# Performance work log

Measured on AMD Instinct MI355X. Metric: run time of the kernel, lower is better.

## Reference

```python
import jax, jax.numpy as jnp
import numpy as np

N_GRAPHS = 512  # number of graphs in the batch (static for segment_sum)


def _gcn_norm(edge_index, n_nodes):
    # PyG GCNConv default: add self-loops, symmetric normalization D^-1/2 (A+I) D^-1/2
    loop = jnp.arange(n_nodes, dtype=edge_index.dtype)
    row = jnp.concatenate([edge_index[0], loop])  # source nodes
    col = jnp.concatenate([edge_index[1], loop])  # target nodes
    deg = jax.ops.segment_sum(jnp.ones_like(col, dtype=jnp.float32), col,
                              num_segments=n_nodes)
    dinv = jnp.where(deg > 0, jax.lax.rsqrt(jnp.maximum(deg, 1.0)), 0.0)
    norm = dinv[row] * dinv[col]  # [E + N]
    return row, col, norm


def _gcn_conv(x, row, col, norm, W, b):
    n_nodes = x.shape[0]
    h = x @ W                                   # [N, H] transform first (small GEMM)
    msg = h[row] * norm[:, None]                # gather + scale: [E+N, H]
    out = jax.ops.segment_sum(msg, col, num_segments=n_nodes)  # scatter-add
    return out + b


def _global_mean_pool(h, batch, n_graphs):
    sums = jax.ops.segment_sum(h, batch, num_segments=n_graphs)
    cnt = jax.ops.segment_sum(jnp.ones((h.shape[0],), h.dtype), batch,
                              num_segments=n_graphs)
    return sums / jnp.maximum(cnt, 1.0)[:, None]


def setup_inputs() -> dict:
    key = jax.random.key(0)
    ks = jax.random.split(key, 12)
    N, E, D, H, G, F = 100000, 1600000, 128, 128, N_GRAPHS, 1
    s_in = 1.0 / np.sqrt(D)
    s_h = 1.0 / np.sqrt(H)
    s_5h = 1.0 / np.sqrt(5 * H)
    return {
        "x": jax.random.normal(ks[0], (N, D), dtype=jnp.float32),
        "edge_index": jax.random.randint(ks[1], (2, E), 0, N, dtype=jnp.int64
                                         if jax.config.jax_enable_x64 else jnp.int32),
        "batch": jnp.sort(jax.random.randint(ks[2], (N,), 0, G, dtype=jnp.int64
                                             if jax.config.jax_enable_x64 else jnp.int32)),
        "W1": jax.random.normal(ks[3], (D, H), jnp.float32) * s_in,
        "b1": jnp.zeros((H,), jnp.float32),
        "W2": jax.random.normal(ks[4], (H, H), jnp.float32) * s_h,
        "b2": jnp.zeros((H,), jnp.float32),
        "W3": jax.random.normal(ks[5], (H, H), jnp.float32) * s_h,
        "b3": jnp.zeros((H,), jnp.float32),
        "W4": jax.random.normal(ks[6], (H, H), jnp.float32) * s_h,
        "b4": jnp.zeros((H,), jnp.float32),
        "Wl1": jax.random.normal(ks[7], (5 * H, 5 * H), jnp.float32) * s_5h,
        "bl1": jnp.zeros((5 * H,), jnp.float32),
        "Wl2": jax.random.normal(ks[8], (5 * H, F), jnp.float32) * s_5h,
        "bl2": jnp.zeros((F,), jnp.float32),
    }


def reference(x, edge_index, batch, W1, b1, W2, b2, W3, b3, W4, b4,
              Wl1, bl1, Wl2, bl2):
    n_nodes = x.shape[0]
    row, col, norm = _gcn_norm(edge_index, n_nodes)
    h1 = jax.nn.relu(_gcn_conv(x, row, col, norm, W1, b1))
    h2 = jax.nn.relu(_gcn_conv(h1, row, col, norm, W2, b2))
    h3 = jax.nn.relu(_gcn_conv(h2, row, col, norm, W3, b3))
    h4 = jax.nn.relu(_gcn_conv(h3, row, col, norm, W4, b4))
    # NOTE: source applies conv4 twice (h5 uses self.conv4); conv5 is unused.
    h5 = jax.nn.relu(_gcn_conv(h4, row, col, norm, W4, b4))
    p = jnp.concatenate([
        _global_mean_pool(h1, batch, N_GRAPHS),
        _global_mean_pool(h2, batch, N_GRAPHS),
        _global_mean_pool(h3, batch, N_GRAPHS),
        _global_mean_pool(h4, batch, N_GRAPHS),
        _global_mean_pool(h5, batch, N_GRAPHS),
    ], axis=1)                                   # [G, 5H]
    h = jax.nn.relu(p @ Wl1 + bl1)
    # dropout p=0.5 is identity in eval mode
    h = h @ Wl2 + bl2                            # [G, F]
    return h.reshape(-1)
```

## Files before the change

kernel.cpp:

```cpp
#include <hip/hip_runtime.h>
#include <hip/hip_fp16.h>

#define HID 128

__device__ __forceinline__ float bf2f(unsigned short u) {
    union { unsigned int i; float f; } v;
    v.i = ((unsigned int)u) << 16;
    return v.f;
}
__device__ __forceinline__ unsigned short f2bf(float f) {
    union { float f; unsigned int i; } v;
    v.f = f;
    unsigned int lsb = (v.i >> 16) & 1u;
    v.i += 0x7fffu + lsb;
    return (unsigned short)(v.i >> 16);
}

template <int S>
__device__ __forceinline__ float fp8_dec(unsigned int v) {
#if __has_builtin(__builtin_amdgcn_cvt_f32_fp8)
    return __builtin_amdgcn_cvt_f32_fp8(v, S);
#else
    unsigned int b = (v >> (S * 8)) & 0xffu;
    unsigned short u = (unsigned short)(((b & 0x80u) << 8) | ((b & 0x7fu) << 7));
    return __half2float(__ushort_as_half(u)) * 256.0f;
#endif
}
__device__ __forceinline__ unsigned char fp8_enc(float f) {
    f = fminf(fmaxf(f, -448.f), 448.f);
    unsigned short u = __half_as_ushort(__float2half(f * 0.00390625f));
    unsigned short r = (unsigned short)(u + (((u >> 7) & 1u) + 0x3fu));
    return (unsigned char)(((r >> 7) & 0x7fu) | ((u >> 8) & 0x80u));
}

typedef __attribute__((ext_vector_type(8))) short bf16x8;
typedef __attribute__((ext_vector_type(4))) float f32x4;

__global__ void k_prep(const int* __restrict__ col, int* __restrict__ degI,
                       int* __restrict__ rank,
                       const float* __restrict__ W1, const float* __restrict__ W2,
                       const float* __restrict__ W3, const float* __restrict__ W4,
                       unsigned short* __restrict__ Wg,
                       const int* __restrict__ batch, int* __restrict__ gstart,
                       int E, int N, int G, int degGrid) {
    int bid = blockIdx.x;
    if (bid < degGrid) {
        int i = bid * 256 + threadIdx.x;
        if (i < E) rank[i] = atomicAdd(&degI[col[i]], 1);
        return;
    }
    bid -= degGrid;
    if (bid < 256) {
        int m = bid >> 6;
        int i = (bid & 63) * 256 + threadIdx.x;
        const float* Wm = (m == 0) ? W1 : (m == 1) ? W2 : (m == 2) ? W3 : W4;
        int k = i >> 7, n = i & 127;
        int ks = k >> 5, q = (k >> 3) & 3, j = k & 7;
        int ct = n >> 4, c = n & 15;
        Wg[m * 16384 + ((((ks * 8 + ct) * 4 + q) * 16 + c) << 3) + j] = f2bf(Wm[i]);
        return;
    }
    bid -= 256;
    int g = bid * 256 + threadIdx.x;
    if (g > G) return;
    int lo = 0, hi = N;
    while (lo < hi) {
        int mid = (lo + hi) >> 1;
        if (batch[mid] < g) lo = mid + 1; else hi = mid;
    }
    gstart[g] = lo;
}

__global__ void k_scan_part(const int* __restrict__ degI, int* __restrict__ partial,
                            int* __restrict__ sums, int N) {
    __shared__ int sh[1024];
    int tid = threadIdx.x;
    int i = blockIdx.x * 1024 + tid;
    int v = (i < N) ? (degI[i] + 1) : 0;
    sh[tid] = v;
    __syncthreads();
    for (int off = 1; off < 1024; off <<= 1) {
        int t = (tid >= off) ? sh[tid - off] : 0;
        __syncthreads();
        sh[tid] += t;
        __syncthreads();
    }
    if (i < N) partial[i] = sh[tid] - v;
    if (tid == 1023) sums[blockIdx.x] = sh[1023];
}
__global__ void k_scan_tops(int* __restrict__ sums, int* __restrict__ indptr,
                            int nblocks, int N) {
    __shared__ int sh[1024];
    int tid = threadIdx.x;
    int v = (tid < nblocks) ? sums[tid] : 0;
    sh[tid] = v;
    __syncthreads();
    for (int off = 1; off < 1024; off <<= 1) {
        int t = (tid >= off) ? sh[tid - off] : 0;
        __syncthreads();
        sh[tid] += t;
        __syncthreads();
    }
    if (tid < nblocks) sums[tid] = sh[tid] - v;
    if (tid == 1023) indptr[N] = sh[1023];
}
__global__ void k_scan_fix(const int* __restrict__ partial, const int* __restrict__ sums,
                           const int* __restrict__ degI, int* __restrict__ indptr,
                           float* __restrict__ dinv, int N) {
    int i = blockIdx.x * blockDim.x + threadIdx.x;
    if (i < N) {
        indptr[i] = partial[i] + sums[i >> 10];
        dinv[i] = 1.0f / sqrtf((float)(degI[i] + 1));
    }
}

__device__ __forceinline__ bf16x8 a_frag_load(const unsigned short* p) {
    return *(const bf16x8*)p;
}
__device__ __forceinline__ bf16x8 a_frag_load(const float* p) {
    bf16x8 r;
#pragma unroll
    for (int i = 0; i < 8; ++i) r[i] = (short)f2bf(p[i]);
    return r;
}

template <typename TA>
__device__ __forceinline__ void gemm_body(const TA* __restrict__ A,
                                          const unsigned short* __restrict__ B,
                                          unsigned char* __restrict__ C,
                                          int N, int blk) {
    const int tid = threadIdx.x;
    const int lane = tid & 63, wave = tid >> 6;
    const int q = lane >> 4, c = lane & 15;
    const int rowBase = blk * 128 + wave * 32;

    f32x4 acc[2][8];
#pragma unroll
    for (int rt = 0; rt < 2; ++rt)
#pragma unroll
        for (int ct = 0; ct < 8; ++ct)
            acc[rt][ct] = (f32x4){0.f, 0.f, 0.f, 0.f};

    const bf16x8 zfrag = {};
#pragma unroll
    for (int ks = 0; ks < 4; ++ks) {
        bf16x8 a[2];
#pragma unroll
        for (int rt = 0; rt < 2; ++rt) {
            int r = rowBase + rt * 16 + c;
            a[rt] = (r < N) ? a_frag_load(A + (size_t)r * HID + ks * 32 + q * 8)
                            : zfrag;
        }
#pragma unroll
        for (int ct = 0; ct < 8; ++ct) {
            bf16x8 b = *(const bf16x8*)&B[((((ks * 8 + ct) * 4 + q) * 16 + c) << 3)];
            acc[0][ct] = __builtin_amdgcn_mfma_f32_16x16x32_bf16(a[0], b, acc[0][ct], 0, 0, 0);
            acc[1][ct] = __builtin_amdgcn_mfma_f32_16x16x32_bf16(a[1], b, acc[1][ct], 0, 0, 0);
        }
    }
#pragma unroll
    for (int rt = 0; rt < 2; ++rt)
#pragma unroll
        for (int reg = 0; reg < 4; ++reg) {
            int r = rowBase + rt * 16 + q * 4 + reg;
            if (r < N) {
#pragma unroll
                for (int ct = 0; ct < 8; ++ct)
                    C[(size_t)r * HID + ct * 16 + c] = fp8_enc(acc[rt][ct][reg]);
            }
        }
}

__device__ __forceinline__ void pool_body(const unsigned short* __restrict__ h,
                                          const int* __restrict__ gstart,
                                          float* __restrict__ pbuf,
                                          int layer, int g, int lane) {
    int s = gstart[g], e = gstart[g + 1];
    float sx[4] = {0.f, 0.f, 0.f, 0.f};
    float sy[4] = {0.f, 0.f, 0.f, 0.f};
    int v = s;
    for (; v + 7 < e; v += 8) {
        unsigned int pk[8];
#pragma unroll
        for (int u = 0; u < 8; ++u)
            pk[u] = ((const unsigned int*)(h + (size_t)(v + u) * HID))[lane];
#pragma unroll
        for (int u = 0; u < 8; ++u) {
            sx[u & 3] += bf2f((unsigned short)(pk[u] & 0xffffu));
            sy[u & 3] += bf2f((unsigned short)(pk[u] >> 16));
        }
    }
    for (; v < e; ++v) {
        unsigned int pk = ((const unsigned int*)(h + (size_t)v * HID))[lane];
        sx[0] += bf2f((unsigned short)(pk & 0xffffu));
        sy[0] += bf2f((unsigned short)(pk >> 16));
    }
    float inv = 1.0f / fmaxf((float)(e - s), 1.0f);
    float ox = ((sx[0] + sx[1]) + (sx[2] + sx[3])) * inv;
    float oy = ((sy[0] + sy[1]) + (sy[2] + sy[3])) * inv;
    float* dst = pbuf + (size_t)g * 640 + layer * HID + lane * 2;
    dst[0] = ox;
    dst[1] = oy;
}

__global__ __launch_bounds__(256) void k_fused0(const float* __restrict__ x,
                                                const unsigned short* __restrict__ Wg,
                                                unsigned char* __restrict__ buf0,
                                                const int* __restrict__ row,
                                                const int* __restrict__ col,
                                                const float* __restrict__ dinv,
                                                const int* __restrict__ indptr,
                                                const int* __restrict__ rank,
                                                int2* __restrict__ adj,
                                                int E, int N, int gemmGrid) {
    __shared__ unsigned short Wsw[16384];
    if (blockIdx.x < gemmGrid) {
        const uint4* src = (const uint4*)Wg;
        uint4* dst = (uint4*)Wsw;
        for (int i = threadIdx.x; i < 2048; i += 256) dst[i] = src[i];
        __syncthreads();
        gemm_body<float>(x, Wsw, buf0, N, blockIdx.x);
        return;
    }
    int e = (blockIdx.x - gemmGrid) * blockDim.x + threadIdx.x;
    if (e >= E + N) return;
    int s, d, p;
    if (e < E) { s = row[e]; d = col[e]; p = indptr[d] + rank[e]; }
    else       { s = d = e - E; p = indptr[d + 1] - 1; }
    adj[p] = make_int2(s, __float_as_int(dinv[s] * dinv[d]));
}

__global__ __launch_bounds__(256) void k_gemm_pool(const unsigned short* __restrict__ A,
                                                   const unsigned short* __restrict__ Wg,
                                                   unsigned char* __restrict__ C,
                                                   int N,
                                                   const int* __restrict__ gstart,
                                                   float* __restrict__ pbuf,
                                                   int poolLayer, int G, int gemmGrid) {
    if (blockIdx.x < gemmGrid) {
        gemm_body<unsigned short>(A, Wg, C, N, blockIdx.x);
        return;
    }
    int g = (blockIdx.x - gemmGrid) * 4 + (threadIdx.x >> 6);
    if (g >= G) return;
    pool_body(A, gstart, pbuf, poolLayer, g, threadIdx.x & 63);
}

__global__ __launch_bounds__(256) void k_aggregate(const unsigned char* __restrict__ t,
                                                   const int* __restrict__ indptr,
                                                   const int2* __restrict__ adj,
                                                   const float* __restrict__ bias,
                                                   unsigned short* __restrict__ h, int N) {
    int node = blockIdx.x * 16 + (threadIdx.x >> 4);
    if (node >= N) return;
    int fl = threadIdx.x & 15;
    int s = indptr[node], e = indptr[node + 1];
    const uint2* tu8 = (const uint2*)t;

    float a0 = 0.f, a1 = 0.f, a2 = 0.f, a3 = 0.f;
    float a4 = 0.f, a5 = 0.f, a6 = 0.f, a7 = 0.f;

    int p = s;
    for (; p + 7 < e; p += 8) {
        uint2 v[8];
        float w[8];
#pragma unroll
        for (int u = 0; u < 8; ++u) {
            int2 ae = adj[p + u];
            w[u] = __int_as_float(ae.y);
            v[u] = tu8[(size_t)ae.x * 16 + fl];
        }
#pragma unroll
        for (int u = 0; u < 8; ++u) {
            a0 = fmaf(w[u], fp8_dec<0>(v[u].x), a0);
            a1 = fmaf(w[u], fp8_dec<1>(v[u].x), a1);
            a2 = fmaf(w[u], fp8_dec<2>(v[u].x), a2);
            a3 = fmaf(w[u], fp8_dec<3>(v[u].x), a3);
            a4 = fmaf(w[u], fp8_dec<0>(v[u].y), a4);
            a5 = fmaf(w[u], fp8_dec<1>(v[u].y), a5);
            a6 = fmaf(w[u], fp8_dec<2>(v[u].y), a6);
            a7 = fmaf(w[u], fp8_dec<3>(v[u].y), a7);
        }
    }
    if (p < e) {
        uint2 v[8];
        float w[8];
#pragma unroll
        for (int u = 0; u < 8; ++u) {
            int idx = p + u;
            int2 ae = adj[idx < e ? idx : e - 1];
            w[u] = (idx < e) ? __int_as_float(ae.y) : 0.f;
            v[u] = tu8[(size_t)ae.x * 16 + fl];
        }
#pragma unroll
        for (int u = 0; u < 8; ++u) {
            a0 = fmaf(w[u], fp8_dec<0>(v[u].x), a0);
            a1 = fmaf(w[u], fp8_dec<1>(v[u].x), a1);
            a2 = fmaf(w[u], fp8_dec<2>(v[u].x), a2);
            a3 = fmaf(w[u], fp8_dec<3>(v[u].x), a3);
            a4 = fmaf(w[u], fp8_dec<0>(v[u].y), a4);
            a5 = fmaf(w[u], fp8_dec<1>(v[u].y), a5);
            a6 = fmaf(w[u], fp8_dec<2>(v[u].y), a6);
            a7 = fmaf(w[u], fp8_dec<3>(v[u].y), a7);
        }
    }
    int fb = fl * 8;
    float4 b0 = *(const float4*)(bias + fb);
    float4 b1 = *(const float4*)(bias + fb + 4);
    uint4 pk;
    pk.x = (unsigned int)f2bf(fmaxf(a0 + b0.x, 0.f)) |
           ((unsigned int)f2bf(fmaxf(a1 + b0.y, 0.f)) << 16);
    pk.y = (unsigned int)f2bf(fmaxf(a2 + b0.z, 0.f)) |
           ((unsigned int)f2bf(fmaxf(a3 + b0.w, 0.f)) << 16);
    pk.z = (unsigned int)f2bf(fmaxf(a4 + b1.x, 0.f)) |
           ((unsigned int)f2bf(fmaxf(a5 + b1.y, 0.f)) << 16);
    pk.w = (unsigned int)f2bf(fmaxf(a6 + b1.z, 0.f)) |
           ((unsigned int)f2bf(fmaxf(a7 + b1.w, 0.f)) << 16);
    ((uint4*)(h + (size_t)node * HID))[fl] = pk;
}

__global__ __launch_bounds__(256) void k_pool(const unsigned short* __restrict__ h,
                                              const int* __restrict__ gstart,
                                              float* __restrict__ pbuf,
                                              int layer, int G) {
    int g = blockIdx.x * 4 + (threadIdx.x >> 6);
    if (g >= G) return;
    pool_body(h, gstart, pbuf, layer, g, threadIdx.x & 63);
}

__global__ __launch_bounds__(256) void k_head1(const float* __restrict__ P,
                                               const float* __restrict__ Wl1,
                                               const float* __restrict__ bl1,
                                               float* __restrict__ Z, int G) {
    __shared__ float As[64][68];
    __shared__ float Ws[64][64];
    const int tid = threadIdx.x;
    const int tr = tid >> 4;
    const int tc = tid & 15;
    const int gBase = blockIdx.x * 64;
    const int cBase = blockIdx.y * 64;

    float acc[4][4];
#pragma unroll
    for (int i = 0; i < 4; ++i)
#pragma unroll
        for (int j = 0; j < 4; ++j) acc[i][j] = 0.f;

    for (int kb = 0; kb < 640; kb += 64) {
#pragma unroll
        for (int i = 0; i < 4; ++i) {
            int f4 = tid + i * 256;
            int r  = f4 >> 4;
            int kc = (f4 & 15) << 2;
            int gg = gBase + r;
            float4 v = {0.f, 0.f, 0.f, 0.f};
            if (gg < G) v = *(const float4*)(P + (size_t)gg * 640 + kb + kc);
            As[kc + 0][r] = v.x; As[kc + 1][r] = v.y;
            As[kc + 2][r] = v.z; As[kc + 3][r] = v.w;
        }
#pragma unroll
        for (int i = 0; i < 4; ++i) {
            int f4 = tid + i * 256;
            int k  = f4 >> 4;
            int c4 = (f4 & 15) << 2;
            *(float4*)&Ws[k][c4] =
                *(const float4*)(Wl1 + (size_t)(kb + k) * 640 + cBase + c4);
        }
        __syncthreads();
#pragma unroll
        for (int k = 0; k < 64; ++k) {
            float a[4], w[4];
            *(float4*)&a[0] = *(const float4*)&As[k][tr * 4];
            *(float4*)&w[0] = *(const float4*)&Ws[k][tc * 4];
#pragma unroll
            for (int i = 0; i < 4; ++i)
#pragma unroll
                for (int j = 0; j < 4; ++j)
                    acc[i][j] = fmaf(a[i], w[j], acc[i][j]);
        }
        __syncthreads();
    }
#pragma unroll
    for (int i = 0; i < 4; ++i) {
        int gg = gBase + tr * 4 + i;
        if (gg < G) {
            float4 o;
            o.x = fmaxf(acc[i][0] + bl1[cBase + tc * 4 + 0], 0.f);
            o.y = fmaxf(acc[i][1] + bl1[cBase + tc * 4 + 1], 0.f);
            o.z = fmaxf(acc[i][2] + bl1[cBase + tc * 4 + 2], 0.f);
            o.w = fmaxf(acc[i][3] + bl1[cBase + tc * 4 + 3], 0.f);
            *(float4*)(Z + (size_t)gg * 640 + cBase + tc * 4) = o;
        }
    }
}

__global__ void k_fc2(const float* __restrict__ zbuf, const float* __restrict__ Wl2,
                      const float* __restrict__ bl2, float* __restrict__ out) {
    int g = blockIdx.x;
    int t = threadIdx.x;
    float s = 0.f;
    for (int k = t; k < 640; k += 128) s = fmaf(zbuf[(size_t)g * 640 + k], Wl2[k], s);
#pragma unroll
    for (int off = 32; off > 0; off >>= 1) s += __shfl_down(s, off);
    __shared__ float ws[2];
    if ((t & 63) == 0) ws[t >> 6] = s;
    __syncthreads();
    if (t == 0) out[g] = ws[0] + ws[1] + bl2[0];
}

extern "C" void kernel_launch(void* const* d_in, const int* in_sizes, int n_in,
                              void* d_out, int out_size, void* d_ws, size_t ws_size,
                              hipStream_t stream) {
    const float* x    = (const float*)d_in[0];
    const int*   edge = (const int*)d_in[1];
    const int*   bat  = (const int*)d_in[2];
    const float* W1   = (const float*)d_in[3];
    const float* b1   = (const float*)d_in[4];
    const float* W2   = (const float*)d_in[5];
    const float* b2   = (const float*)d_in[6];
    const float* W3   = (const float*)d_in[7];
    const float* b3   = (const float*)d_in[8];
    const float* W4   = (const float*)d_in[9];
    const float* b4   = (const float*)d_in[10];
    const float* Wl1  = (const float*)d_in[11];
    const float* bl1  = (const float*)d_in[12];
    const float* Wl2  = (const float*)d_in[13];
    const float* bl2  = (const float*)d_in[14];
    float*       out  = (float*)d_out;

    const int N = in_sizes[2];
    const int E = in_sizes[1] / 2;
    const int G = out_size;
    (void)n_in; (void)ws_size;

    (void)hipGetLastError();

    size_t off = 0;
    auto alloc = [&](size_t bytes) -> void* {
        void* p = (void*)((char*)d_ws + off);
        off += (bytes + 255) & ~(size_t)255;
        return p;
    };
    unsigned char*  buf0 = (unsigned char*)alloc((size_t)N * HID);
    unsigned short* buf1 = (unsigned short*)alloc((size_t)N * HID * 2);
    unsigned short* Wg   = (unsigned short*)alloc((size_t)4 * 16384 * 2);
    float* dinv   = (float*)alloc((size_t)N * 4);
    int*   degI   = (int*)alloc((size_t)N * 4);
    int*   rank   = (int*)alloc((size_t)E * 4);
    int*   indptr = (int*)alloc((size_t)(N + 1) * 4);
    int*   partial= (int*)alloc((size_t)N * 4);
    int*   bsums  = (int*)alloc((size_t)1024 * 4);
    int2*  adj    = (int2*)alloc((size_t)(E + N) * 8);
    int*   gstart = (int*)alloc((size_t)(G + 1) * 4);
    float* pbuf   = (float*)alloc((size_t)G * 640 * 4);
    float* zbuf   = (float*)alloc((size_t)G * 640 * 4);

    const int* rowv = edge;
    const int* colv = edge + E;

    hipMemsetAsync(degI, 0, (size_t)N * 4, stream);
    const int degGrid = (E + 255) / 256;
    const int gbGrid  = (G + 256) / 256;
    k_prep<<<degGrid + 256 + gbGrid, 256, 0, stream>>>(colv, degI, rank,
                                                       W1, W2, W3, W4, Wg,
                                                       bat, gstart,
                                                       E, N, G, degGrid);
    const int scanBlocks = (N + 1023) / 1024;
    k_scan_part<<<scanBlocks, 1024, 0, stream>>>(degI, partial, bsums, N);
    k_scan_tops<<<1, 1024, 0, stream>>>(bsums, indptr, scanBlocks, N);
    k_scan_fix<<<(N + 255) / 256, 256, 0, stream>>>(partial, bsums, degI,
                                                    indptr, dinv, N);

    const int gemmGrid = (N + 127) / 128;
    const int scatGrid = (E + N + 255) / 256;
    k_fused0<<<gemmGrid + scatGrid, 256, 0, stream>>>(x, Wg, buf0, rowv, colv,
                                                      dinv, indptr, rank, adj,
                                                      E, N, gemmGrid);

    const int aggGrid  = (N + 15) / 16;
    const int poolGrid = (G + 3) / 4;

    k_aggregate<<<aggGrid, 256, 0, stream>>>(buf0, indptr, adj, b1, buf1, N);
    const float* bs_[4] = {b2, b3, b4, b4};
    const int Wi_[4] = {1, 2, 3, 3};
    for (int i = 0; i < 4; ++i) {
        k_gemm_pool<<<gemmGrid + poolGrid, 256, 0, stream>>>(
            buf1, Wg + Wi_[i] * 16384, buf0, N, gstart, pbuf, i, G, gemmGrid);
        k_aggregate<<<aggGrid, 256, 0, stream>>>(buf0, indptr, adj, bs_[i], buf1, N);
    }
    k_pool<<<poolGrid, 256, 0, stream>>>(buf1, gstart, pbuf, 4, G);

    dim3 hgrid((G + 63) / 64, 10);
    k_head1<<<hgrid, 256, 0, stream>>>(pbuf, Wl1, bl1, zbuf, G);
    k_fc2<<<G, 128, 0, stream>>>(zbuf, Wl2, bl2, out);

    if (hipGetLastError() != hipSuccess)
        hipMemsetAsync(d_out, 0x42, (size_t)out_size * 4, stream);
}
```

Measured before the change: 608.7 us.

## Move first GEMM into prep kernel and widen aggregate loads to 16 bytes

The layer-1 GEMM now runs inside the prep kernel alongside degree counting. Each GEMM block converts W1 into swizzled bf16 in shared memory itself rather than waiting for the Wg copy, and the edge scatter becomes its own kernel. The aggregate kernel now uses 8 lanes per node with 16-byte fp8 gathers and 16 accumulators, where it previously used 16 lanes with 8-byte gathers. This aims to overlap the GEMM with the atomic degree pass and to cut load instructions per gathered row. The trade-offs are that every GEMM block repeats the W1 conversion, and the aggregate uses more registers while giving each node fewer lanes.

```diff
diff --git a/kernel.cpp b/kernel.cpp
--- a/kernel.cpp
+++ b/kernel.cpp
@@ -36,13 +36,72 @@
 typedef __attribute__((ext_vector_type(8))) short bf16x8;
 typedef __attribute__((ext_vector_type(4))) float f32x4;
 
-__global__ void k_prep(const int* __restrict__ col, int* __restrict__ degI,
-                       int* __restrict__ rank,
-                       const float* __restrict__ W1, const float* __restrict__ W2,
-                       const float* __restrict__ W3, const float* __restrict__ W4,
-                       unsigned short* __restrict__ Wg,
-                       const int* __restrict__ batch, int* __restrict__ gstart,
-                       int E, int N, int G, int degGrid) {
+__device__ __forceinline__ bf16x8 a_frag_load(const unsigned short* p) {
+    return *(const bf16x8*)p;
+}
+__device__ __forceinline__ bf16x8 a_frag_load(const float* p) {
+    bf16x8 r;
+#pragma unroll
+    for (int i = 0; i < 8; ++i) r[i] = (short)f2bf(p[i]);
+    return r;
+}
+
+template <typename TA>
+__device__ __forceinline__ void gemm_body(const TA* __restrict__ A,
+                                          const unsigned short* __restrict__ B,
+                                          unsigned char* __restrict__ C,
+                                          int N, int blk) {
+    const int tid = threadIdx.x;
+    const int lane = tid & 63, wave = tid >> 6;
+    const int q = lane >> 4, c = lane & 15;
+    const int rowBase = blk * 128 + wave * 32;
+
+    f32x4 acc[2][8];
+#pragma unroll
+    for (int rt = 0; rt < 2; ++rt)
+#pragma unroll
+        for (int ct = 0; ct < 8; ++ct)
+            acc[rt][ct] = (f32x4){0.f, 0.f, 0.f, 0.f};
+
+    const bf16x8 zfrag = {};
+#pragma unroll
+    for (int ks = 0; ks < 4; ++ks) {
+        bf16x8 a[2];
+#pragma unroll
+        for (int rt = 0; rt < 2; ++rt) {
+            int r = rowBase + rt * 16 + c;
+            a[rt] = (r < N) ? a_frag_load(A + (size_t)r * HID + ks * 32 + q * 8)
+                            : zfrag;
+        }
+#pragma unroll
+        for (int ct = 0; ct < 8; ++ct) {
+            bf16x8 b = *(const bf16x8*)&B[((((ks * 8 + ct) * 4 + q) * 16 + c) << 3)];
+            acc[0][ct] = __builtin_amdgcn_mfma_f32_16x16x32_bf16(a[0], b, acc[0][ct], 0, 0, 0);
+            acc[1][ct] = __builtin_amdgcn_mfma_f32_16x16x32_bf16(a[1], b, acc[1][ct], 0, 0, 0);
+        }
+    }
+#pragma unroll
+    for (int rt = 0; rt < 2; ++rt)
+#pragma unroll
+        for (int reg = 0; reg < 4; ++reg) {
+            int r = rowBase + rt * 16 + q * 4 + reg;
+            if (r < N) {
+#pragma unroll
+                for (int ct = 0; ct < 8; ++ct)
+                    C[(size_t)r * HID + ct * 16 + c] = fp8_enc(acc[rt][ct][reg]);
+            }
+        }
+}
+
+__global__ __launch_bounds__(256) void k_prep_gemm(
+        const int* __restrict__ col, int* __restrict__ degI, int* __restrict__ rank,
+        const float* __restrict__ x, const float* __restrict__ W1,
+        unsigned char* __restrict__ buf0,
+        const float* __restrict__ W2, const float* __restrict__ W3,
+        const float* __restrict__ W4, unsigned short* __restrict__ Wg,
+        const int* __restrict__ batch, int* __restrict__ gstart,
+        int E, int N, int G, int degGrid, int gemmGrid) {
+    __shared__ unsigned short Wsw[16384];
     int bid = blockIdx.x;
     if (bid < degGrid) {
         int i = bid * 256 + threadIdx.x;
@@ -50,6 +109,20 @@
         return;
     }
     bid -= degGrid;
+    if (bid < gemmGrid) {
+#pragma unroll 4
+        for (int tt = 0; tt < 64; ++tt) {
+            int i = tt * 256 + threadIdx.x;
+            int k = i >> 7, n = i & 127;
+            int ks = k >> 5, q = (k >> 3) & 3, j = k & 7;
+            int ct = n >> 4, c = n & 15;
+            Wsw[((((ks * 8 + ct) * 4 + q) * 16 + c) << 3) + j] = f2bf(W1[i]);
+        }
+        __syncthreads();
+        gemm_body<float>(x, Wsw, buf0, N, bid);
+        return;
+    }
+    bid -= gemmGrid;
     if (bid < 256) {
         int m = bid >> 6;
         int i = (bid & 63) * 256 + threadIdx.x;
@@ -114,61 +187,19 @@
     }
 }
 
-__device__ __forceinline__ bf16x8 a_frag_load(const unsigned short* p) {
-    return *(const bf16x8*)p;
-}
-__device__ __forceinline__ bf16x8 a_frag_load(const float* p) {
-    bf16x8 r;
-#pragma unroll
-    for (int i = 0; i < 8; ++i) r[i] = (short)f2bf(p[i]);
-    return r;
-}
-
-template <typename TA>
-__device__ __forceinline__ void gemm_body(const TA* __restrict__ A,
-                                          const unsigned short* __restrict__ B,
-                                          unsigned char* __restrict__ C,
-                                          int N, int blk) {
-    const int tid = threadIdx.x;
-    const int lane = tid & 63, wave = tid >> 6;
-    const int q = lane >> 4, c = lane & 15;
-    const int rowBase = blk * 128 + wave * 32;
-
-    f32x4 acc[2][8];
-#pragma unroll
-    for (int rt = 0; rt < 2; ++rt)
-#pragma unroll
-        for (int ct = 0; ct < 8; ++ct)
-            acc[rt][ct] = (f32x4){0.f, 0.f, 0.f, 0.f};
-
-    const bf16x8 zfrag = {};
-#pragma unroll
-    for (int ks = 0; ks < 4; ++ks) {
-        bf16x8 a[2];
-#pragma unroll
-        for (int rt = 0; rt < 2; ++rt) {
-            int r = rowBase + rt * 16 + c;
-            a[rt] = (r < N) ? a_frag_load(A + (size_t)r * HID + ks * 32 + q * 8)
-                            : zfrag;
-        }
-#pragma unroll
-        for (int ct = 0; ct < 8; ++ct) {
-            bf16x8 b = *(const bf16x8*)&B[((((ks * 8 + ct) * 4 + q) * 16 + c) << 3)];
-            acc[0][ct] = __builtin_amdgcn_mfma_f32_16x16x32_bf16(a[0], b, acc[0][ct], 0, 0, 0);
-            acc[1][ct] = __builtin_amdgcn_mfma_f32_16x16x32_bf16(a[1], b, acc[1][ct], 0, 0, 0);
-        }
-    }
-#pragma unroll
-    for (int rt = 0; rt < 2; ++rt)
-#pragma unroll
-        for (int reg = 0; reg < 4; ++reg) {
-            int r = rowBase + rt * 16 + q * 4 + reg;
-            if (r < N) {
-#pragma unroll
-                for (int ct = 0; ct < 8; ++ct)
-                    C[(size_t)r * HID + ct * 16 + c] = fp8_enc(acc[rt][ct][reg]);
-            }
-        }
+__global__ __launch_bounds__(256) void k_scat(const int* __restrict__ row,
+                                              const int* __restrict__ col,
+                                              const float* __restrict__ dinv,
+                                              const int* __restrict__ indptr,
+                                              const int* __restrict__ rank,
+                                              int2* __restrict__ adj,
+                                              int E, int N) {
+    int e = blockIdx.x * blockDim.x + threadIdx.x;
+    if (e >= E + N) return;
+    int s, d, p;
+    if (e < E) { s = row[e]; d = col[e]; p = indptr[d] + rank[e]; }
+    else       { s = d = e - E; p = indptr[d + 1] - 1; }
+    adj[p] = make_int2(s, __float_as_int(dinv[s] * dinv[d]));
 }
 
 __device__ __forceinline__ void pool_body(const unsigned short* __restrict__ h,
@@ -203,33 +234,6 @@
     dst[1] = oy;
 }
 
-__global__ __launch_bounds__(256) void k_fused0(const float* __restrict__ x,
-                                                const unsigned short* __restrict__ Wg,
-                                                unsigned char* __restrict__ buf0,
-                                                const int* __restrict__ row,
-                                                const int* __restrict__ col,
-                                                const float* __restrict__ dinv,
-                                                const int* __restrict__ indptr,
-                                                const int* __restrict__ rank,
-                                                int2* __restrict__ adj,
-                                                int E, int N, int gemmGrid) {
-    __shared__ unsigned short Wsw[16384];
-    if (blockIdx.x < gemmGrid) {
-        const uint4* src = (const uint4*)Wg;
-        uint4* dst = (uint4*)Wsw;
-        for (int i = threadIdx.x; i < 2048; i += 256) dst[i] = src[i];
-        __syncthreads();
-        gemm_body<float>(x, Wsw, buf0, N, blockIdx.x);
-        return;
-    }
-    int e = (blockIdx.x - gemmGrid) * blockDim.x + threadIdx.x;
-    if (e >= E + N) return;
-    int s, d, p;
-    if (e < E) { s = row[e]; d = col[e]; p = indptr[d] + rank[e]; }
-    else       { s = d = e - E; p = indptr[d + 1] - 1; }
-    adj[p] = make_int2(s, __float_as_int(dinv[s] * dinv[d]));
-}
-
 __global__ __launch_bounds__(256) void k_gemm_pool(const unsigned short* __restrict__ A,
                                                    const unsigned short* __restrict__ Wg,
                                                    unsigned char* __restrict__ C,
@@ -251,72 +255,103 @@
                                                    const int2* __restrict__ adj,
                                                    const float* __restrict__ bias,
                                                    unsigned short* __restrict__ h, int N) {
-    int node = blockIdx.x * 16 + (threadIdx.x >> 4);
+    int node = blockIdx.x * 32 + (threadIdx.x >> 3);
     if (node >= N) return;
-    int fl = threadIdx.x & 15;
+    int fl = threadIdx.x & 7;
     int s = indptr[node], e = indptr[node + 1];
-    const uint2* tu8 = (const uint2*)t;
-
-    float a0 = 0.f, a1 = 0.f, a2 = 0.f, a3 = 0.f;
-    float a4 = 0.f, a5 = 0.f, a6 = 0.f, a7 = 0.f;
+    const uint4* tu16 = (const uint4*)t;
+
+    float a[16];
+#pragma unroll
+    for (int i = 0; i < 16; ++i) a[i] = 0.f;
 
     int p = s;
     for (; p + 7 < e; p += 8) {
-        uint2 v[8];
+        uint4 v[8];
         float w[8];
 #pragma unroll
         for (int u = 0; u < 8; ++u) {
             int2 ae = adj[p + u];
             w[u] = __int_as_float(ae.y);
-            v[u] = tu8[(size_t)ae.x * 16 + fl];
+            v[u] = tu16[(size_t)ae.x * 8 + fl];
         }
 #pragma unroll
         for (int u = 0; u < 8; ++u) {
-            a0 = fmaf(w[u], fp8_dec<0>(v[u].x), a0);
-            a1 = fmaf(w[u], fp8_dec<1>(v[u].x), a1);
-            a2 = fmaf(w[u], fp8_dec<2>(v[u].x), a2);
-            a3 = fmaf(w[u], fp8_dec<3>(v[u].x), a3);
-            a4 = fmaf(w[u], fp8_dec<0>(v[u].y), a4);
-            a5 = fmaf(w[u], fp8_dec<1>(v[u].y), a5);
-            a6 = fmaf(w[u], fp8_dec<2>(v[u].y), a6);
-            a7 = fmaf(w[u], fp8_dec<3>(v[u].y), a7);
+            a[0]  = fmaf(w[u], fp8_dec<0>(v[u].x), a[0]);
+            a[1]  = fmaf(w[u], fp8_dec<1>(v[u].x), a[1]);
+            a[2]  = fmaf(w[u], fp8_dec<2>(v[u].x), a[2]);
+            a[3]  = fmaf(w[u], fp8_dec<3>(v[u].x), a[3]);
+            a[4]  = fmaf(w[u], fp8_dec<0>(v[u].y), a[4]);
+            a[5]  = fmaf(w[u], fp8_dec<1>(v[u].y), a[5]);
+            a[6]  = fmaf(w[u], fp8_dec<2>(v[u].y), a[6]);
+            a[7]  = fmaf(w[u], fp8_dec<3>(v[u].y), a[7]);
+            a[8]  = fmaf(w[u], fp8_dec<0>(v[u].z), a[8]);
+            a[9]  = fmaf(w[u], fp8_dec<1>(v[u].z), a[9]);
+            a[10] = fmaf(w[u], fp8_dec<2>(v[u].z), a[10]);
+            a[11] = fmaf(w[u], fp8_dec<3>(v[u].z), a[11]);
+            a[12] = fmaf(w[u], fp8_dec<0>(v[u].w), a[12]);
+            a[13] = fmaf(w[u], fp8_dec<1>(v[u].w), a[13]);
+            a[14] = fmaf(w[u], fp8_dec<2>(v[u].w), a[14]);
+            a[15] = fmaf(w[u], fp8_dec<3>(v[u].w), a[15]);
         }
     }
     if (p < e) {
-        uint2 v[8];
+        uint4 v[8];
         float w[8];
 #pragma unroll
         for (int u = 0; u < 8; ++u) {
             int idx = p + u;
             int2 ae = adj[idx < e ? idx : e - 1];
             w[u] = (idx < e) ? __int_as_float(ae.y) : 0.f;
-            v[u] = tu8[(size_t)ae.x * 16 + fl];
+            v[u] = tu16[(size_t)ae.x * 8 + fl];
         }
 #pragma unroll
         for (int u = 0; u < 8; ++u) {
-            a0 = fmaf(w[u], fp8_dec<0>(v[u].x), a0);
-            a1 = fmaf(w[u], fp8_dec<1>(v[u].x), a1);
-            a2 = fmaf(w[u], fp8_dec<2>(v[u].x), a2);
-            a3 = fmaf(w[u], fp8_dec<3>(v[u].x), a3);
-            a4 = fmaf(w[u], fp8_dec<0>(v[u].y), a4);
-            a5 = fmaf(w[u], fp8_dec<1>(v[u].y), a5);
-            a6 = fmaf(w[u], fp8_dec<2>(v[u].y), a6);
-            a7 = fmaf(w[u], fp8_dec<3>(v[u].y), a7);
-        }
-    }
-    int fb = fl * 8;
-    float4 b0 = *(const float4*)(bias + fb);
-    float4 b1 = *(const float4*)(bias + fb + 4);
-    uint4 pk;
-    pk.x = (unsigned int)f2bf(fmaxf(a0 + b0.x, 0.f)) |
-           ((unsigned int)f2bf(fmaxf(a1 + b0.y, 0.f)) << 16);
-    pk.y = (unsigned int)f2bf(fmaxf(a2 + b0.z, 0.f)) |
-           ((unsigned int)f2bf(fmaxf(a3 + b0.w, 0.f)) << 16);
-    pk.z = (unsigned int)f2bf(fmaxf(a4 + b1.x, 0.f)) |
-           ((unsigned int)f2bf(fmaxf(a5 + b1.y, 0.f)) << 16);
-    pk.w = (unsigned int)f2bf(fmaxf(a6 + b1.z, 0.f)) |
-           ((unsigned int)f2bf(fmaxf(a7 + b1.w, 0.f)) << 16);
-    ((uint4*)(h + (size_t)node * HID))[fl] = pk;
+            a[0]  = fmaf(w[u], fp8_dec<0>(v[u].x), a[0]);
+            a[1]  = fmaf(w[u], fp8_dec<1>(v[u].x), a[1]);
+            a[2]  = fmaf(w[u], fp8_dec<2>(v[u].x), a[2]);
+            a[3]  = fmaf(w[u], fp8_dec<3>(v[u].x), a[3]);
+            a[4]  = fmaf(w[u], fp8_dec<0>(v[u].y), a[4]);
+            a[5]  = fmaf(w[u], fp8_dec<1>(v[u].y), a[5]);
+            a[6]  = fmaf(w[u], fp8_dec<2>(v[u].y), a[6]);
+            a[7]  = fmaf(w[u], fp8_dec<3>(v[u].y), a[7]);
+            a[8]  = fmaf(w[u], fp8_dec<0>(v[u].z), a[8]);
+            a[9]  = fmaf(w[u], fp8_dec<1>(v[u].z), a[9]);
+            a[10] = fmaf(w[u], fp8_dec<2>(v[u].z), a[10]);
+            a[11] = fmaf(w[u], fp8_dec<3>(v[u].z), a[11]);
+            a[12] = fmaf(w[u], fp8_dec<0>(v[u].w), a[12]);
+            a[13] = fmaf(w[u], fp8_dec<1>(v[u].w), a[13]);
+            a[14] = fmaf(w[u], fp8_dec<2>(v[u].w), a[14]);
+            a[15] = fmaf(w[u], fp8_dec<3>(v[u].w), a[15]);
+        }
+    }
+    int fb = fl * 16;
+    uint4 pk0, pk1;
+    {
+        float4 b0 = *(const float4*)(bias + fb);
+        float4 b1 = *(const float4*)(bias + fb + 4);
+        float4 b2 = *(const float4*)(bias + fb + 8);
+        float4 b3 = *(const float4*)(bias + fb + 12);
+        pk0.x = (unsigned int)f2bf(fmaxf(a[0]  + b0.x, 0.f)) |
+                ((unsigned int)f2bf(fmaxf(a[1]  + b0.y, 0.f)) << 16);
+        pk0.y = (unsigned int)f2bf(fmaxf(a[2]  + b0.z, 0.f)) |
+                ((unsigned int)f2bf(fmaxf(a[3]  + b0.w, 0.f)) << 16);
+        pk0.z = (unsigned int)f2bf(fmaxf(a[4]  + b1.x, 0.f)) |
+                ((unsigned int)f2bf(fmaxf(a[5]  + b1.y, 0.f)) << 16);
+        pk0.w = (unsigned int)f2bf(fmaxf(a[6]  + b1.z, 0.f)) |
+                ((unsigned int)f2bf(fmaxf(a[7]  + b1.w, 0.f)) << 16);
+        pk1.x = (unsigned int)f2bf(fmaxf(a[8]  + b2.x, 0.f)) |
+                ((unsigned int)f2bf(fmaxf(a[9]  + b2.y, 0.f)) << 16);
+        pk1.y = (unsigned int)f2bf(fmaxf(a[10] + b2.z, 0.f)) |
+                ((unsigned int)f2bf(fmaxf(a[11] + b2.w, 0.f)) << 16);
+        pk1.z = (unsigned int)f2bf(fmaxf(a[12] + b3.x, 0.f)) |
+                ((unsigned int)f2bf(fmaxf(a[13] + b3.y, 0.f)) << 16);
+        pk1.w = (unsigned int)f2bf(fmaxf(a[14] + b3.z, 0.f)) |
+                ((unsigned int)f2bf(fmaxf(a[15] + b3.w, 0.f)) << 16);
+    }
+    uint4* hp = (uint4*)(h + (size_t)node * HID);
+    hp[fl * 2]     = pk0;
+    hp[fl * 2 + 1] = pk1;
 }
 
 __global__ __launch_bounds__(256) void k_pool(const unsigned short* __restrict__ h,
@@ -459,25 +494,23 @@
     const int* colv = edge + E;
 
     hipMemsetAsync(degI, 0, (size_t)N * 4, stream);
-    const int degGrid = (E + 255) / 256;
-    const int gbGrid  = (G + 256) / 256;
-    k_prep<<<degGrid + 256 + gbGrid, 256, 0, stream>>>(colv, degI, rank,
-                                                       W1, W2, W3, W4, Wg,
-                                                       bat, gstart,
-                                                       E, N, G, degGrid);
+    const int degGrid  = (E + 255) / 256;
+    const int gemmGrid = (N + 127) / 128;
+    const int gbGrid   = (G + 256) / 256;
+    k_prep_gemm<<<degGrid + gemmGrid + 256 + gbGrid, 256, 0, stream>>>(
+        colv, degI, rank, x, W1, buf0, W2, W3, W4, Wg, bat, gstart,
+        E, N, G, degGrid, gemmGrid);
+
     const int scanBlocks = (N + 1023) / 1024;
     k_scan_part<<<scanBlocks, 1024, 0, stream>>>(degI, partial, bsums, N);
     k_scan_tops<<<1, 1024, 0, stream>>>(bsums, indptr, scanBlocks, N);
     k_scan_fix<<<(N + 255) / 256, 256, 0, stream>>>(partial, bsums, degI,
                                                     indptr, dinv, N);
 
-    const int gemmGrid = (N + 127) / 128;
     const int scatGrid = (E + N + 255) / 256;
-    k_fused0<<<gemmGrid + scatGrid, 256, 0, stream>>>(x, Wg, buf0, rowv, colv,
-                                                      dinv, indptr, rank, adj,
-                                                      E, N, gemmGrid);
-
-    const int aggGrid  = (N + 15) / 16;
+    k_scat<<<scatGrid, 256, 0, stream>>>(rowv, colv, dinv, indptr, rank, adj, E, N);
+
+    const int aggGrid  = (N + 31) / 32;
     const int poolGrid = (G + 3) / 4;
 
     k_aggregate<<<aggGrid, 256, 0, stream>>>(buf0, indptr, adj, b1, buf1, N);
```

Result: slower. 669.8 us (+10.0%).
